# Optimization experiments

Measured on AMD Instinct MI355X. Metric: run time of the kernel, lower is better.

Reference implementation:

```python
import jax, jax.numpy as jnp
import numpy as np


def _conv1d(x, kernel, bias):
    # Keras Conv1D, padding='valid', stride 1. x: (b, ts, c); kernel: (K, c, f)
    y = jax.lax.conv_general_dilated(x, kernel, (1,), 'VALID',
                                     dimension_numbers=('NWC', 'WIO', 'NWC'))
    return y + bias


def setup_inputs() -> dict:
    key = jax.random.key(0)
    k1, k2, k3 = jax.random.split(key, 3)
    KSIZE, C, F = 5, 32, 32
    x = jax.random.normal(k1, (16, 65536, C), jnp.float32)
    Wconv = jax.random.normal(k2, (KSIZE, C, F), jnp.float32) * 0.05
    bconv = jnp.zeros((F,), jnp.float32)
    Wdef = jax.random.normal(k3, (KSIZE, 1), jnp.float32) * 0.1
    return {"x": x, "Wconv": Wconv, "bconv": bconv, "Wdef": Wdef}


def reference(x, Wconv, bconv, Wdef):
    K = Wconv.shape[0]
    # regularGrid: R = [-floor(K/2), ..., K-1-floor(K/2)]
    R = jnp.arange(K, dtype=jnp.float32) - (K // 2)
    offset = _conv1d(x, Wconv, bconv)                 # (b, ts-K+1, f)
    # dpn = mean over all positions of (offset + R) -> mean(offset) + R, shape (K,)
    pn = jnp.mean(offset) + R
    # g(Q, Q+pn) = max(0, 1 - |Q - (Q+pn)|) = max(0, 1 - |pn|): constant per tap
    scale = jnp.maximum(0.0, 1.0 - jnp.abs(pn))       # (K,)
    # y_k = scale_k * flatten(x); sum_k W_k * y_k == x * sum_k(W_k * scale_k)
    s = jnp.sum(Wdef[:, 0] * scale)                   # scalar
    y = x * s                                         # (b, ts, c)
    return _conv1d(y, Wconv, bconv)                   # (b, ts-K+1, f)
```

## Files before the change

kernel.cpp:

```cpp
#include <hip/hip_runtime.h>
#include <hip/hip_fp16.h>

#define T    65536
#define TOUT 65532
#define NB   16
#define CH   32
#define NF   32
#define KS   5
#define BM   128
#define NCHB 2048

typedef _Float16 f16x8 __attribute__((ext_vector_type(8)));
typedef _Float16 f16x4 __attribute__((ext_vector_type(4)));
typedef float    f32x4 __attribute__((ext_vector_type(4)));


__device__ __forceinline__ f16x4 cvt4(float4 v) {
    f16x4 h;
    h[0] = (_Float16)v.x; h[1] = (_Float16)v.y;
    h[2] = (_Float16)v.z; h[3] = (_Float16)v.w;
    return h;
}

__global__ __launch_bounds__(256) void chsum3_kernel(const float* __restrict__ x,
                                                     float* __restrict__ partials) {
    __shared__ float tot[CH];
    const int tid = threadIdx.x;
    if (tid < CH) tot[tid] = 0.f;
    __syncthreads();

    const float4* x4 = (const float4*)x;
    const size_t idx4 = (size_t)blockIdx.x * 256 + tid;
    float s0 = 0.f, s1 = 0.f, s2 = 0.f, s3 = 0.f;
#pragma unroll
    for (int q = 0; q < 16; ++q) {
        float4 v = x4[idx4 + (size_t)q * (NCHB * 256)];
        s0 += v.x; s1 += v.y; s2 += v.z; s3 += v.w;
    }
    const int c0 = (tid & 7) * 4;
    atomicAdd(&tot[c0 + 0], s0);
    atomicAdd(&tot[c0 + 1], s1);
    atomicAdd(&tot[c0 + 2], s2);
    atomicAdd(&tot[c0 + 3], s3);
    __syncthreads();
    if (tid < CH) partials[(size_t)blockIdx.x * CH + tid] = tot[tid];
}

__global__ __launch_bounds__(256) void scalar2_kernel(const float* __restrict__ x,
                                                      const float* __restrict__ Wconv,
                                                      const float* __restrict__ bconv,
                                                      const float* __restrict__ Wdef,
                                                      const float* __restrict__ partials,
                                                      float* __restrict__ ws) {
    __shared__ float ltot[CH];
    __shared__ float hb[4][CH], tb[4][CH];
    __shared__ float partial[256];
    const int tid = threadIdx.x;
    if (tid < CH) ltot[tid] = 0.f;
    __syncthreads();

    {
        const float4* p4 = (const float4*)partials;
        float s0 = 0.f, s1 = 0.f, s2 = 0.f, s3 = 0.f;
#pragma unroll 8
        for (int i = 0; i < 64; ++i) {
            float4 v = p4[i * 256 + tid];
            s0 += v.x; s1 += v.y; s2 += v.z; s3 += v.w;
        }
        int c0 = (tid & 7) * 4;
        atomicAdd(&ltot[c0 + 0], s0);
        atomicAdd(&ltot[c0 + 1], s1);
        atomicAdd(&ltot[c0 + 2], s2);
        atomicAdd(&ltot[c0 + 3], s3);
    }
    {
        int j = tid >> 5, c = tid & 31;
        int row = (j < 4) ? j : (T - 8 + j);
        float e = 0.f;
        for (int bb = 0; bb < NB; ++bb)
            e += x[((size_t)bb * T + row) * CH + c];
        if (j < 4) hb[j][c] = e; else tb[j - 4][c] = e;
    }
    __syncthreads();

    float term = 0.f;
    if (tid < KS * CH) {
        int k = tid >> 5, c = tid & 31;
        float wf = 0.f;
        const float* wp = &Wconv[(size_t)tid * NF];
        for (int f = 0; f < NF; ++f) wf += wp[f];
        float S = ltot[c];
        for (int jj = 0; jj < k; ++jj) S -= hb[jj][c];
        for (int jj = k; jj < 4; ++jj) S -= tb[jj][c];
        term = wf * S;
    }
    partial[tid] = term;
    __syncthreads();
    for (int off = 128; off > 0; off >>= 1) {
        if (tid < off) partial[tid] += partial[tid + off];
        __syncthreads();
    }
    if (tid == 0) {
        float sum_b = 0.f;
        for (int f = 0; f < NF; ++f) sum_b += bconv[f];
        float mean_off = partial[0] / (float)((size_t)NB * TOUT * NF) + sum_b / (float)NF;
        float s = 0.f;
        for (int k = 0; k < KS; ++k) {
            float pn = mean_off + (float)(k - 2);
            s += Wdef[k] * fmaxf(0.f, 1.f - fabsf(pn));
        }
        ws[CH] = s;
    }
}

__global__ __launch_bounds__(256) void conv_kernel(const float* __restrict__ x,
                                                   const float* __restrict__ Wconv,
                                                   const float* __restrict__ bconv,
                                                   const float* __restrict__ ws,
                                                   float* __restrict__ out) {
    __shared__ _Float16 A[(BM + 4) * 40];
    __shared__ _Float16 Wt[KS * CH * 40];

    int tid = threadIdx.x;
    int b   = blockIdx.y;
    int t0  = blockIdx.x * BM;

    const int AROWS = BM + 4;
    {
        int c0 = (tid & 7) * 4;
        for (int r = (tid >> 3); r < AROWS; r += 32) {
            int t = t0 + r;
            float4 v = make_float4(0.f, 0.f, 0.f, 0.f);
            if (t < T) v = *(const float4*)&x[((size_t)b * T + t) * CH + c0];
            *(f16x4*)&A[r * 40 + c0] = cvt4(v);
        }
    }
    if (tid < KS * CH) {
        int k = tid >> 5, c = tid & 31;
        const float* wp = &Wconv[(size_t)tid * NF];
        for (int f = 0; f < NF; ++f)
            Wt[(k * CH + f) * 40 + c] = (_Float16)wp[f];
    }
    __syncthreads();

    int lane = tid & 63;
    int wave = tid >> 6;
    int rowbase = wave * 32;
    int lrow = lane & 15;
    int kgrp = lane >> 4;

    f32x4 acc00 = {}, acc01 = {}, acc10 = {}, acc11 = {};
#pragma unroll
    for (int kk = 0; kk < KS; ++kk) {
        f16x8 a0 = *(const f16x8*)&A[(rowbase + lrow + kk) * 40 + kgrp * 8];
        f16x8 a1 = *(const f16x8*)&A[(rowbase + 16 + lrow + kk) * 40 + kgrp * 8];
        f16x8 b0 = *(const f16x8*)&Wt[(kk * CH + lrow) * 40 + kgrp * 8];
        f16x8 b1 = *(const f16x8*)&Wt[(kk * CH + 16 + lrow) * 40 + kgrp * 8];
        acc00 = __builtin_amdgcn_mfma_f32_16x16x32_f16(a0, b0, acc00, 0, 0, 0);
        acc01 = __builtin_amdgcn_mfma_f32_16x16x32_f16(a0, b1, acc01, 0, 0, 0);
        acc10 = __builtin_amdgcn_mfma_f32_16x16x32_f16(a1, b0, acc10, 0, 0, 0);
        acc11 = __builtin_amdgcn_mfma_f32_16x16x32_f16(a1, b1, acc11, 0, 0, 0);
    }

    float sv  = ws[CH];
    int col0  = lane & 15;
    float bc0 = bconv[col0], bc1 = bconv[col0 + 16];
    int rbase = rowbase + ((lane >> 4) << 2);
#pragma unroll
    for (int reg = 0; reg < 4; ++reg) {
        int t = t0 + rbase + reg;
        if (t < TOUT) {
            float* o = &out[((size_t)b * TOUT + t) * NF];
            o[col0]      = sv * acc00[reg] + bc0;
            o[col0 + 16] = sv * acc01[reg] + bc1;
        }
        int t1 = t + 16;
        if (t1 < TOUT) {
            float* o = &out[((size_t)b * TOUT + t1) * NF];
            o[col0]      = sv * acc10[reg] + bc0;
            o[col0 + 16] = sv * acc11[reg] + bc1;
        }
    }
}

extern "C" void kernel_launch(void* const* d_in, const int* in_sizes, int n_in,
                              void* d_out, int out_size, void* d_ws, size_t ws_size,
                              hipStream_t stream) {
    const float* x     = (const float*)d_in[0];
    const float* Wconv = (const float*)d_in[1];
    const float* bconv = (const float*)d_in[2];
    const float* Wdef  = (const float*)d_in[3];
    float* out      = (float*)d_out;
    float* ws       = (float*)d_ws;
    float* partials = ws + 64;

    chsum3_kernel<<<dim3(NCHB), dim3(256), 0, stream>>>(x, partials);
    scalar2_kernel<<<dim3(1), dim3(256), 0, stream>>>(x, Wconv, bconv, Wdef, partials, ws);
    dim3 grid((TOUT + BM - 1) / BM, NB);
    conv_kernel<<<grid, dim3(256), 0, stream>>>(x, Wconv, bconv, ws, out);
}
```

Measured before the change: 88.88 us.

## Emit fp16 copy of input during channel-sum pass and convolve from it

The reduction pass now also writes a half-precision copy of x into workspace. The convolution kernel then loads that copy instead of re-reading and converting fp32 x. The reduction uses wave shuffles before the shared atomics, and the weight transpose is vectorised. The intent is to halve the conv kernel's input bytes, at the cost of an extra 64 MiB write in the first pass. The old path is kept as a fallback when the workspace is too small.

Measured after the change: 86.56 us. 1.03x faster.

```diff
diff --git a/kernel.cpp b/kernel.cpp
--- a/kernel.cpp
+++ b/kernel.cpp
@@ -13,8 +13,15 @@
 typedef _Float16 f16x8 __attribute__((ext_vector_type(8)));
 typedef _Float16 f16x4 __attribute__((ext_vector_type(4)));
 typedef float    f32x4 __attribute__((ext_vector_type(4)));
-
-
+typedef float    f32x4v __attribute__((ext_vector_type(4)));
+
+
+__device__ __forceinline__ f16x4 cvt4v(f32x4v v) {
+    f16x4 h;
+    h[0] = (_Float16)v[0]; h[1] = (_Float16)v[1];
+    h[2] = (_Float16)v[2]; h[3] = (_Float16)v[3];
+    return h;
+}
 __device__ __forceinline__ f16x4 cvt4(float4 v) {
     f16x4 h;
     h[0] = (_Float16)v.x; h[1] = (_Float16)v.y;
@@ -22,26 +29,40 @@
     return h;
 }
 
-__global__ __launch_bounds__(256) void chsum3_kernel(const float* __restrict__ x,
+__global__ __launch_bounds__(256) void chsum4_kernel(const float* __restrict__ x,
+                                                     _Float16* __restrict__ xh,
                                                      float* __restrict__ partials) {
     __shared__ float tot[CH];
-    const int tid = threadIdx.x;
+    const int tid  = threadIdx.x;
+    const int lane = tid & 63;
     if (tid < CH) tot[tid] = 0.f;
     __syncthreads();
 
-    const float4* x4 = (const float4*)x;
+    const f32x4v* x4  = (const f32x4v*)x;
+    f16x4*        xh4 = (f16x4*)xh;
     const size_t idx4 = (size_t)blockIdx.x * 256 + tid;
     float s0 = 0.f, s1 = 0.f, s2 = 0.f, s3 = 0.f;
 #pragma unroll
     for (int q = 0; q < 16; ++q) {
-        float4 v = x4[idx4 + (size_t)q * (NCHB * 256)];
-        s0 += v.x; s1 += v.y; s2 += v.z; s3 += v.w;
-    }
-    const int c0 = (tid & 7) * 4;
-    atomicAdd(&tot[c0 + 0], s0);
-    atomicAdd(&tot[c0 + 1], s1);
-    atomicAdd(&tot[c0 + 2], s2);
-    atomicAdd(&tot[c0 + 3], s3);
+        size_t i = idx4 + (size_t)q * (NCHB * 256);
+        f32x4v v = __builtin_nontemporal_load(&x4[i]);
+        s0 += v[0]; s1 += v[1]; s2 += v[2]; s3 += v[3];
+        xh4[i] = cvt4v(v);
+    }
+#pragma unroll
+    for (int m = 8; m <= 32; m <<= 1) {
+        s0 += __shfl_xor(s0, m, 64);
+        s1 += __shfl_xor(s1, m, 64);
+        s2 += __shfl_xor(s2, m, 64);
+        s3 += __shfl_xor(s3, m, 64);
+    }
+    if (lane < 8) {
+        const int c0 = lane * 4;
+        atomicAdd(&tot[c0 + 0], s0);
+        atomicAdd(&tot[c0 + 1], s1);
+        atomicAdd(&tot[c0 + 2], s2);
+        atomicAdd(&tot[c0 + 3], s3);
+    }
     __syncthreads();
     if (tid < CH) partials[(size_t)blockIdx.x * CH + tid] = tot[tid];
 }
@@ -58,7 +79,6 @@
     const int tid = threadIdx.x;
     if (tid < CH) ltot[tid] = 0.f;
     __syncthreads();
-
     {
         const float4* p4 = (const float4*)partials;
         float s0 = 0.f, s1 = 0.f, s2 = 0.f, s3 = 0.f;
@@ -113,41 +133,50 @@
     }
 }
 
-__global__ __launch_bounds__(256) void conv_kernel(const float* __restrict__ x,
-                                                   const float* __restrict__ Wconv,
-                                                   const float* __restrict__ bconv,
-                                                   const float* __restrict__ ws,
-                                                   float* __restrict__ out) {
+__global__ __launch_bounds__(256) void conv2_kernel(const _Float16* __restrict__ xh,
+                                                    const float* __restrict__ Wconv,
+                                                    const float* __restrict__ bconv,
+                                                    const float* __restrict__ ws,
+                                                    float* __restrict__ out) {
     __shared__ _Float16 A[(BM + 4) * 40];
     __shared__ _Float16 Wt[KS * CH * 40];
 
-    int tid = threadIdx.x;
-    int b   = blockIdx.y;
-    int t0  = blockIdx.x * BM;
-
-    const int AROWS = BM + 4;
-    {
-        int c0 = (tid & 7) * 4;
-        for (int r = (tid >> 3); r < AROWS; r += 32) {
+    const int tid = threadIdx.x;
+    const int b   = blockIdx.y;
+    const int t0  = blockIdx.x * BM;
+    const int c0  = (tid & 7) * 4;
+
+    {
+        const f16x4* xh4 = (const f16x4*)xh;
+        for (int r = (tid >> 3); r < BM + 4; r += 32) {
             int t = t0 + r;
-            float4 v = make_float4(0.f, 0.f, 0.f, 0.f);
-            if (t < T) v = *(const float4*)&x[((size_t)b * T + t) * CH + c0];
-            *(f16x4*)&A[r * 40 + c0] = cvt4(v);
-        }
-    }
-    if (tid < KS * CH) {
-        int k = tid >> 5, c = tid & 31;
-        const float* wp = &Wconv[(size_t)tid * NF];
-        for (int f = 0; f < NF; ++f)
-            Wt[(k * CH + f) * 40 + c] = (_Float16)wp[f];
-    }
-    __syncthreads();
-
-    int lane = tid & 63;
-    int wave = tid >> 6;
-    int rowbase = wave * 32;
-    int lrow = lane & 15;
-    int kgrp = lane >> 4;
+            f16x4 h = {};
+            if (t < T) h = xh4[((size_t)b * T + t) * 8 + (tid & 7)];
+            *(f16x4*)&A[r * 40 + c0] = h;
+        }
+    }
+    {
+        const float4* w4 = (const float4*)Wconv;
+#pragma unroll
+        for (int j = 0; j < 5; ++j) {
+            int i4 = tid + j * 256;
+            float4 v = w4[i4];
+            int fi = i4 * 4;
+            int k = fi >> 10, c = (fi >> 5) & 31, f = fi & 31;
+            _Float16* wrow = &Wt[(k * CH + f) * 40 + c];
+            wrow[0 * 40] = (_Float16)v.x;
+            wrow[1 * 40] = (_Float16)v.y;
+            wrow[2 * 40] = (_Float16)v.z;
+            wrow[3 * 40] = (_Float16)v.w;
+        }
+    }
+    __syncthreads();
+
+    const int lane = tid & 63;
+    const int wave = tid >> 6;
+    const int rowbase = wave * 32;
+    const int lrow = lane & 15;
+    const int kgrp = lane >> 4;
 
     f32x4 acc00 = {}, acc01 = {}, acc10 = {}, acc11 = {};
 #pragma unroll
@@ -162,6 +191,93 @@
         acc11 = __builtin_amdgcn_mfma_f32_16x16x32_f16(a1, b1, acc11, 0, 0, 0);
     }
 
+    float sv  = ws[CH];
+    int col0  = lane & 15;
+    float bc0 = bconv[col0], bc1 = bconv[col0 + 16];
+    int rbase = rowbase + ((lane >> 4) << 2);
+#pragma unroll
+    for (int reg = 0; reg < 4; ++reg) {
+        int t = t0 + rbase + reg;
+        if (t < TOUT) {
+            float* o = &out[((size_t)b * TOUT + t) * NF];
+            o[col0]      = sv * acc00[reg] + bc0;
+            o[col0 + 16] = sv * acc01[reg] + bc1;
+        }
+        int t1 = t + 16;
+        if (t1 < TOUT) {
+            float* o = &out[((size_t)b * TOUT + t1) * NF];
+            o[col0]      = sv * acc10[reg] + bc0;
+            o[col0 + 16] = sv * acc11[reg] + bc1;
+        }
+    }
+}
+
+__global__ __launch_bounds__(256) void chsum3_kernel(const float* __restrict__ x,
+                                                     float* __restrict__ partials) {
+    __shared__ float tot[CH];
+    const int tid = threadIdx.x;
+    if (tid < CH) tot[tid] = 0.f;
+    __syncthreads();
+    const float4* x4 = (const float4*)x;
+    const size_t idx4 = (size_t)blockIdx.x * 256 + tid;
+    float s0 = 0.f, s1 = 0.f, s2 = 0.f, s3 = 0.f;
+#pragma unroll
+    for (int q = 0; q < 16; ++q) {
+        float4 v = x4[idx4 + (size_t)q * (NCHB * 256)];
+        s0 += v.x; s1 += v.y; s2 += v.z; s3 += v.w;
+    }
+    const int c0 = (tid & 7) * 4;
+    atomicAdd(&tot[c0 + 0], s0);
+    atomicAdd(&tot[c0 + 1], s1);
+    atomicAdd(&tot[c0 + 2], s2);
+    atomicAdd(&tot[c0 + 3], s3);
+    __syncthreads();
+    if (tid < CH) partials[(size_t)blockIdx.x * CH + tid] = tot[tid];
+}
+
+__global__ __launch_bounds__(256) void conv_kernel(const float* __restrict__ x,
+                                                   const float* __restrict__ Wconv,
+                                                   const float* __restrict__ bconv,
+                                                   const float* __restrict__ ws,
+                                                   float* __restrict__ out) {
+    __shared__ _Float16 A[(BM + 4) * 40];
+    __shared__ _Float16 Wt[KS * CH * 40];
+    int tid = threadIdx.x;
+    int b   = blockIdx.y;
+    int t0  = blockIdx.x * BM;
+    {
+        int c0 = (tid & 7) * 4;
+        for (int r = (tid >> 3); r < BM + 4; r += 32) {
+            int t = t0 + r;
+            float4 v = make_float4(0.f, 0.f, 0.f, 0.f);
+            if (t < T) v = *(const float4*)&x[((size_t)b * T + t) * CH + c0];
+            *(f16x4*)&A[r * 40 + c0] = cvt4(v);
+        }
+    }
+    if (tid < KS * CH) {
+        int k = tid >> 5, c = tid & 31;
+        const float* wp = &Wconv[(size_t)tid * NF];
+        for (int f = 0; f < NF; ++f)
+            Wt[(k * CH + f) * 40 + c] = (_Float16)wp[f];
+    }
+    __syncthreads();
+    int lane = tid & 63;
+    int wave = tid >> 6;
+    int rowbase = wave * 32;
+    int lrow = lane & 15;
+    int kgrp = lane >> 4;
+    f32x4 acc00 = {}, acc01 = {}, acc10 = {}, acc11 = {};
+#pragma unroll
+    for (int kk = 0; kk < KS; ++kk) {
+        f16x8 a0 = *(const f16x8*)&A[(rowbase + lrow + kk) * 40 + kgrp * 8];
+        f16x8 a1 = *(const f16x8*)&A[(rowbase + 16 + lrow + kk) * 40 + kgrp * 8];
+        f16x8 b0 = *(const f16x8*)&Wt[(kk * CH + lrow) * 40 + kgrp * 8];
+        f16x8 b1 = *(const f16x8*)&Wt[(kk * CH + 16 + lrow) * 40 + kgrp * 8];
+        acc00 = __builtin_amdgcn_mfma_f32_16x16x32_f16(a0, b0, acc00, 0, 0, 0);
+        acc01 = __builtin_amdgcn_mfma_f32_16x16x32_f16(a0, b1, acc01, 0, 0, 0);
+        acc10 = __builtin_amdgcn_mfma_f32_16x16x32_f16(a1, b0, acc10, 0, 0, 0);
+        acc11 = __builtin_amdgcn_mfma_f32_16x16x32_f16(a1, b1, acc11, 0, 0, 0);
+    }
     float sv  = ws[CH];
     int col0  = lane & 15;
     float bc0 = bconv[col0], bc1 = bconv[col0 + 16];
@@ -193,9 +309,18 @@
     float* out      = (float*)d_out;
     float* ws       = (float*)d_ws;
     float* partials = ws + 64;
-
-    chsum3_kernel<<<dim3(NCHB), dim3(256), 0, stream>>>(x, partials);
-    scalar2_kernel<<<dim3(1), dim3(256), 0, stream>>>(x, Wconv, bconv, Wdef, partials, ws);
+    _Float16* xh    = (_Float16*)((char*)d_ws + 524288);
+
+    const size_t need = 524288 + (size_t)NB * T * CH * sizeof(_Float16);
     dim3 grid((TOUT + BM - 1) / BM, NB);
-    conv_kernel<<<grid, dim3(256), 0, stream>>>(x, Wconv, bconv, ws, out);
-}
+
+    if (ws_size >= need) {
+        chsum4_kernel<<<dim3(NCHB), dim3(256), 0, stream>>>(x, xh, partials);
+        scalar2_kernel<<<dim3(1), dim3(256), 0, stream>>>(x, Wconv, bconv, Wdef, partials, ws);
+        conv2_kernel<<<grid, dim3(256), 0, stream>>>(xh, Wconv, bconv, ws, out);
+    } else {
+        chsum3_kernel<<<dim3(NCHB), dim3(256), 0, stream>>>(x, partials);
+        scalar2_kernel<<<dim3(1), dim3(256), 0, stream>>>(x, Wconv, bconv, Wdef, partials, ws);
+        conv_kernel<<<grid, dim3(256), 0, stream>>>(x, Wconv, bconv, ws, out);
+    }
+}
```
